# Optimization experiments

Measured on AMD Instinct MI355X. Metric: run time of the kernel, lower is better.

The kernel has to match this reference:

```python
import jax, jax.numpy as jnp
import numpy as np

B, H, W, C = 2, 64, 64, 96
DIN, NST, RNK, K = 192, 16, 6, 4
L = H * W


def _make_ids():
    idx = np.arange(L).reshape(H, W)
    p0 = idx.reshape(-1)
    p1 = idx.T.reshape(-1)
    p2 = p0[::-1].copy()
    p3 = p1[::-1].copy()
    scan = np.stack([p0, p1, p2, p3]).astype(np.int32)
    inv = np.stack([np.argsort(p) for p in scan]).astype(np.int32)
    return jnp.asarray(scan), jnp.asarray(inv)


def setup_inputs() -> dict:
    key = jax.random.key(0)
    ks = jax.random.split(key, 10)
    scan_ids, inv_ids = _make_ids()
    std = RNK ** -0.5
    # dt bias init: inverse-softplus of dt ~ LogUniform(1e-3, 1e-1), as in VMM.dt_init
    u = jax.random.uniform(ks[5], (K, DIN))
    dt = jnp.exp(u * (np.log(0.1) - np.log(0.001)) + np.log(0.001))
    dt_b = dt + jnp.log(-jnp.expm1(-dt))
    return {
        "x": jax.random.normal(ks[0], (B, H, W, C), jnp.float32),
        "W_in": jax.random.normal(ks[1], (2 * DIN, C), jnp.float32) * 0.02,
        "conv_w": jax.random.normal(ks[2], (DIN, 1, 3, 3), jnp.float32) * 0.1,
        "conv_b": jnp.zeros((DIN,), jnp.float32),
        "x_proj_w": jax.random.normal(ks[3], (K, RNK + 2 * NST, DIN), jnp.float32) * 0.02,
        "dt_w": jax.random.uniform(ks[4], (K, DIN, RNK), jnp.float32, -std, std),
        "dt_b": dt_b.astype(jnp.float32),
        "A_logs": jnp.log(jnp.tile(jnp.arange(1, NST + 1, dtype=jnp.float32)[None], (K * DIN, 1))),
        "Ds": jnp.ones((K * DIN,), jnp.float32),
        "gate_w": jax.random.normal(ks[6], (4 * DIN, 4), jnp.float32) * 0.1,  # grouped 1x1 conv, groups=DIN
        "gate_b": jnp.zeros((4 * DIN,), jnp.float32),
        "ln_g": jnp.ones((DIN,), jnp.float32),
        "ln_b": jnp.zeros((DIN,), jnp.float32),
        "W_out": jax.random.normal(ks[7], (C, DIN), jnp.float32) * 0.02,
        "scan_ids": scan_ids,
        "inv_ids": inv_ids,
    }


def _forward(x, W_in, conv_w, conv_b, x_proj_w, dt_w, dt_b, A_logs, Ds, gate_w, gate_b, ln_g, ln_b, W_out, scan_ids, inv_ids):
    b, h, w, c = x.shape
    l = h * w
    din = conv_w.shape[0]
    k = x_proj_w.shape[0]
    nst = A_logs.shape[1]
    rnk = dt_w.shape[2]
    # in_proj + split into x / gate z
    xz = x @ W_in.T
    xc, z = jnp.split(xz, 2, axis=-1)
    xc = jnp.transpose(xc, (0, 3, 1, 2))  # (b, din, h, w)
    # depthwise 3x3 conv + SiLU
    xc = jax.lax.conv_general_dilated(
        xc, conv_w, (1, 1), "SAME", feature_group_count=din,
        dimension_numbers=("NCHW", "OIHW", "NCHW")) + conv_b[None, :, None, None]
    xc = jax.nn.silu(xc)
    # multi-directional gather (mair_ids_scan)
    xf = xc.reshape(b, din, l)
    xs = jnp.moveaxis(xf[:, :, scan_ids], 2, 1)  # (b, k, din, l)
    # x_proj (grouped 1x1 conv) -> dt, B, C
    x_dbl = jnp.einsum("bkdl,krd->bkrl", xs, x_proj_w)
    dts, Bs, Cs = jnp.split(x_dbl, [rnk, rnk + nst], axis=2)  # (b,k,rnk,l),(b,k,n,l),(b,k,n,l)
    delta = jax.nn.softplus(jnp.einsum("bkrl,kdr->bkdl", dts, dt_w) + dt_b[None, :, :, None])
    A = -jnp.exp(A_logs).reshape(k, din, nst)
    dA = jnp.exp(delta[..., None] * A[None, :, :, None, :])              # (b,k,d,l,n)
    dBu = (delta * xs)[..., None] * jnp.moveaxis(Bs, 2, 3)[:, :, None]   # (b,k,d,l,n)

    def step(hst, inp):
        da, dbu = inp
        hst = da * hst + dbu
        return hst, hst

    h0 = jnp.zeros((b, k, din, nst), jnp.float32)
    _, hs = jax.lax.scan(step, h0, (jnp.moveaxis(dA, 3, 0), jnp.moveaxis(dBu, 3, 0)))  # (l,b,k,d,n)
    ys = jnp.einsum("lbkdn,bknl->bkdl", hs, Cs) + xs * Ds.reshape(k, din)[None, :, :, None]
    # inverse scatter (mair_ids_inverse) + concat along channels
    y = jax.vmap(lambda yk, ik: yk[..., ik], in_axes=(1, 0), out_axes=1)(ys, inv_ids)
    y = y.reshape(b, k * din, h, w)
    # ShuffleAttn gating: group = din, group_channels = k
    shuf = y.reshape(b, k, din, h, w).transpose(0, 2, 1, 3, 4).reshape(b, k * din, h, w)
    pooled = shuf.mean(axis=(2, 3)).reshape(b, din, k)
    gate = jax.nn.sigmoid(jnp.einsum("bgi,goi->bgo", pooled, gate_w.reshape(din, k, k)) + gate_b.reshape(din, k))
    gate = gate.transpose(0, 2, 1).reshape(b, k * din)  # channel_rearrange
    y = y * gate[:, :, None, None]
    # sum the 4 direction branches
    y = y.reshape(b, k, din, h, w).sum(axis=1)
    y = jnp.transpose(y, (0, 2, 3, 1))  # (b,h,w,din)
    # LayerNorm(d_inner)
    mu = y.mean(-1, keepdims=True)
    var = ((y - mu) ** 2).mean(-1, keepdims=True)
    y = (y - mu) / jnp.sqrt(var + 1e-5) * ln_g + ln_b
    y = y * jax.nn.silu(z)
    return y @ W_out.T


def reference(x, W_in, conv_w, conv_b, x_proj_w, dt_w, dt_b, A_logs, Ds, gate_w, gate_b, ln_g, ln_b, W_out, scan_ids, inv_ids):
    return _forward(x, W_in, conv_w, conv_b, x_proj_w, dt_w, dt_b, A_logs, Ds, gate_w, gate_b, ln_g, ln_b, W_out, scan_ids, inv_ids)
```

## Files before the change

### kernel.cpp

```cpp
#include <hip/hip_runtime.h>
#include <math.h>

#define BB 2
#define CC 96
#define DIN 192
#define NST 16
#define RNK 6
#define KK 4
#define LL 4096
#define RTOT (RNK + 2*NST)


__global__ __launch_bounds__(256) void k_inproj(const float* __restrict__ x,
        const float* __restrict__ W_in, float* __restrict__ xc_pre,
        float* __restrict__ z_silu) {
    __shared__ float lx[96*65];
    __shared__ float wt[48*196];
    int b = blockIdx.y, z = blockIdx.z;
    int l0 = blockIdx.x * 64;
    int t = threadIdx.x;
    for (int i = 0; i < 24; ++i) {
        int e = t + 256*i;
        int l = e / 96, c = e % 96;
        lx[c*65 + l] = x[((size_t)(b*LL + l0 + l))*96 + c];
    }
    int lg = t & 15;
    int og = t >> 4;
    float acc[4][12];
    #pragma unroll
    for (int j = 0; j < 4; ++j)
        #pragma unroll
        for (int q = 0; q < 12; ++q) acc[j][q] = 0.f;
    for (int p = 0; p < 2; ++p) {
        __syncthreads();
        for (int i = 0; i < 36; ++i) {
            int e = t + 256*i;
            int cc = e % 48, oc = e / 48;
            wt[cc*196 + oc] = W_in[((size_t)(z*192 + oc))*96 + p*48 + cc];
        }
        __syncthreads();
        #pragma unroll 2
        for (int cc = 0; cc < 48; ++cc) {
            int c = p*48 + cc;
            float x0 = lx[c*65 + 4*lg + 0];
            float x1 = lx[c*65 + 4*lg + 1];
            float x2 = lx[c*65 + 4*lg + 2];
            float x3 = lx[c*65 + 4*lg + 3];
            const float* wr = &wt[cc*196 + 12*og];
            float4 w0 = *(const float4*)(wr);
            float4 w1 = *(const float4*)(wr + 4);
            float4 w2 = *(const float4*)(wr + 8);
            float wv[12] = {w0.x,w0.y,w0.z,w0.w, w1.x,w1.y,w1.z,w1.w,
                            w2.x,w2.y,w2.z,w2.w};
            #pragma unroll
            for (int q = 0; q < 12; ++q) {
                acc[0][q] += x0*wv[q];
                acc[1][q] += x1*wv[q];
                acc[2][q] += x2*wv[q];
                acc[3][q] += x3*wv[q];
            }
        }
    }
    float* dst = (z == 0) ? xc_pre : z_silu;
    #pragma unroll
    for (int j = 0; j < 4; ++j) {
        int l = l0 + 4*lg + j;
        size_t base = (size_t)(b*LL + l)*DIN + 12*og;
        #pragma unroll
        for (int q = 0; q < 12; ++q) {
            float v = acc[j][q];
            if (z) v = v / (1.f + __expf(-v));
            dst[base + q] = v;
        }
    }
}

__global__ __launch_bounds__(256) void k_conv(const float* __restrict__ xc,
        const float* __restrict__ cw, const float* __restrict__ cb,
        float* __restrict__ out) {
    int gid = blockIdx.x*256 + threadIdx.x;
    int d = gid % DIN;
    int r = gid / DIN;
    int l = r & 4095, b = r >> 12;
    int w = l & 63, h = l >> 6;
    float acc = cb[d];
    #pragma unroll
    for (int dh = -1; dh <= 1; ++dh) {
        int h2 = h + dh;
        bool okh = (h2 >= 0) && (h2 < 64);
        #pragma unroll
        for (int dw = -1; dw <= 1; ++dw) {
            int w2 = w + dw;
            if (okh && w2 >= 0 && w2 < 64)
                acc += xc[((size_t)(b*LL + h2*64 + w2))*DIN + d] * cw[d*9 + (dh+1)*3 + (dw+1)];
        }
    }
    out[((size_t)(b*LL + l))*DIN + d] = acc / (1.f + __expf(-acc));
}

__global__ __launch_bounds__(512) void k_proj(const float* __restrict__ xconv,
        const int* __restrict__ scan_ids, const float* __restrict__ xpw,
        float* __restrict__ dts, float* __restrict__ Bs, float* __restrict__ Cs) {
    __shared__ float lxs[96*65];
    __shared__ float lw[RTOT*96];
    __shared__ float lbc[64*33];
    __shared__ int lsid[64];
    int k = blockIdx.y, b = blockIdx.z;
    int l0 = blockIdx.x * 64;
    int t = threadIdx.x;
    if (t < 64) lsid[t] = scan_ids[k*LL + l0 + t];
    int l = t & 63;
    int rg = __builtin_amdgcn_readfirstlane(t >> 6);
    float acc[5];
    #pragma unroll
    for (int j = 0; j < 5; ++j) acc[j] = 0.f;
    for (int p = 0; p < 2; ++p) {
        __syncthreads();
        for (int i = 0; i < 12; ++i) {
            int e = t + 512*i;
            int dd = e % 96, ll = e / 96;
            lxs[dd*65 + ll] = xconv[((size_t)(b*LL + lsid[ll]))*DIN + p*96 + dd];
        }
        for (int i = 0; i < 8; ++i) {
            int e = t + 512*i;
            if (e < RTOT*96) {
                int r = e / 96, dd = e % 96;
                lw[r*96 + dd] = xpw[(size_t)k*RTOT*DIN + r*DIN + p*96 + dd];
            }
        }
        __syncthreads();
        for (int dd = 0; dd < 96; dd += 4) {
            float x0 = lxs[(dd+0)*65 + l];
            float x1 = lxs[(dd+1)*65 + l];
            float x2 = lxs[(dd+2)*65 + l];
            float x3 = lxs[(dd+3)*65 + l];
            #pragma unroll
            for (int j = 0; j < 5; ++j) {
                int r = rg + 8*j;
                if (r < RTOT) {
                    float4 w = *(const float4*)&lw[r*96 + dd];
                    acc[j] += x0*w.x + x1*w.y + x2*w.z + x3*w.w;
                }
            }
        }
    }
    int bk = b*KK + k;
    #pragma unroll
    for (int j = 0; j < 5; ++j) {
        int r = rg + 8*j;
        if (r < RNK)       dts[((size_t)bk*LL + l0 + l)*8 + r] = acc[j];
        else if (r < RTOT) lbc[l*33 + (r - RNK)] = acc[j];
    }
    __syncthreads();
    size_t rowb = ((size_t)bk*LL + l0)*NST;
    for (int i = 0; i < 2; ++i) {
        int e = t + 512*i;
        int n = e & 15, ll = e >> 4;
        Bs[rowb + ll*NST + n] = lbc[ll*33 + n];
        Cs[rowb + ll*NST + n] = lbc[ll*33 + 16 + n];
    }
}

__global__ __launch_bounds__(384) void k_scan1(const float* __restrict__ xconv,
        const float* __restrict__ Bs, const float* __restrict__ dts,
        const float* __restrict__ dtw, const float* __restrict__ dtb,
        const int* __restrict__ scan_ids, const float* __restrict__ A_logs,
        float* __restrict__ segA, float* __restrict__ segB, int SL) {
    __shared__ float ldel[32*DIN];
    __shared__ float lB[32*NST];
    __shared__ int lsid[256];
    int seg = blockIdx.x, bk = blockIdx.y;
    int b = bk >> 2, k = bk & 3;
    int t = threadIdx.x;
    int half = t & 1, d = t >> 1;
    int l0 = seg * SL;
    for (int i = t; i < SL; i += 384) lsid[i] = scan_ids[k*LL + l0 + i];
    float Av[8];
    {
        const float4* ap = (const float4*)(A_logs + ((k*DIN + d)*NST + half*8));
        float4 a0 = ap[0], a1 = ap[1];
        Av[0]=-__expf(a0.x); Av[1]=-__expf(a0.y); Av[2]=-__expf(a0.z); Av[3]=-__expf(a0.w);
        Av[4]=-__expf(a1.x); Av[5]=-__expf(a1.y); Av[6]=-__expf(a1.z); Av[7]=-__expf(a1.w);
    }
    float Av0 = -__expf(A_logs[(k*DIN + d)*NST]);
    bool okl = true;
    #pragma unroll
    for (int q = 0; q < 8; ++q) {
        float m = (float)(half*8 + q + 1);
        okl = okl && (fabsf(Av[q] - m*Av0) <= 1e-4f*m);
    }
    int fast = __all(okl);
    int dd = t % DIN, li0 = t / DIN;
    float wdt[RNK];
    float bdt = dtb[k*DIN + dd];
    #pragma unroll
    for (int r = 0; r < RNK; ++r) wdt[r] = dtw[(k*DIN + dd)*RNK + r];
    float h[8];
    #pragma unroll
    for (int n = 0; n < 8; ++n) h[n] = 0.f;
    float sumdv = 0.f;
    __syncthreads();
    float xn = xconv[((size_t)(b*LL + lsid[0]))*DIN + d];
    for (int c0 = 0; c0 < SL; c0 += 32) {
        for (int li = li0; li < 32; li += 2) {
            const float* dr = dts + ((size_t)bk*LL + l0 + c0 + li)*8;
            float aa = bdt;
            #pragma unroll
            for (int r = 0; r < RNK; ++r) aa += dr[r]*wdt[r];
            ldel[li*DIN + dd] = fmaxf(aa, 0.f) + __logf(1.f + __expf(-fabsf(aa)));
        }
        for (int e = t; e < 32*NST; e += 384)
            lB[e] = Bs[((size_t)bk*LL + l0 + c0)*NST + e];
        __syncthreads();
        if (fast) {
            for (int li2 = 0; li2 < 32; ++li2) {
                int li = c0 + li2;
                float xv = xn;
                if (li + 1 < SL) xn = xconv[((size_t)(b*LL + lsid[li+1]))*DIN + d];
                float dv = ldel[li2*DIN + d];
                sumdv += dv;
                float dxv = dv * xv;
                float4 b0 = *(const float4*)&lB[li2*NST + half*8];
                float4 b1 = *(const float4*)&lB[li2*NST + half*8 + 4];
                float bb[8] = {b0.x,b0.y,b0.z,b0.w, b1.x,b1.y,b1.z,b1.w};
                float P[8];
                float E1 = __expf(dv * Av0);
                P[0] = E1;       P[1] = E1*E1;   P[2] = P[1]*E1; P[3] = P[1]*P[1];
                P[4] = P[3]*E1;  P[5] = P[2]*P[2]; P[6] = P[5]*E1; P[7] = P[3]*P[3];
                float s = half ? P[7] : 1.0f;
                #pragma unroll
                for (int n = 0; n < 8; ++n)
                    h[n] = (s*P[n])*h[n] + dxv*bb[n];
            }
        } else {
            for (int li2 = 0; li2 < 32; ++li2) {
                int li = c0 + li2;
                float xv = xn;
                if (li + 1 < SL) xn = xconv[((size_t)(b*LL + lsid[li+1]))*DIN + d];
                float dv = ldel[li2*DIN + d];
                sumdv += dv;
                float dxv = dv * xv;
                float4 b0 = *(const float4*)&lB[li2*NST + half*8];
                float4 b1 = *(const float4*)&lB[li2*NST + half*8 + 4];
                float bb[8] = {b0.x,b0.y,b0.z,b0.w, b1.x,b1.y,b1.z,b1.w};
                #pragma unroll
                for (int n = 0; n < 8; ++n) {
                    float e2 = __expf(dv * Av[n]);
                    h[n] = e2*h[n] + dxv*bb[n];
                }
            }
        }
        __syncthreads();
    }
    float a[8];
    #pragma unroll
    for (int n = 0; n < 8; ++n) a[n] = __expf(Av[n]*sumdv);
    size_t base = (((size_t)bk*gridDim.x + seg)*DIN + d)*NST + half*8;
    *(float4*)&segA[base]     = make_float4(a[0],a[1],a[2],a[3]);
    *(float4*)&segA[base + 4] = make_float4(a[4],a[5],a[6],a[7]);
    *(float4*)&segB[base]     = make_float4(h[0],h[1],h[2],h[3]);
    *(float4*)&segB[base + 4] = make_float4(h[4],h[5],h[6],h[7]);
}

__global__ __launch_bounds__(256) void k_scan2(const float* __restrict__ segA,
        const float* __restrict__ segB, float* __restrict__ hinit, int SEGC) {
    int idx = blockIdx.x*256 + threadIdx.x;
    if (idx >= BB*KK*DIN*NST) return;
    int bk = idx / (DIN*NST);
    int dn = idx % (DIN*NST);
    const size_t stride = DIN*NST;
    size_t o = (size_t)bk*SEGC*stride + dn;
    float h = 0.f;
    for (int s = 0; s < SEGC; s += 8) {
        float av[8], bv[8];
        #pragma unroll
        for (int j = 0; j < 8; ++j) {
            av[j] = segA[o + j*stride];
            bv[j] = segB[o + j*stride];
        }
        #pragma unroll
        for (int j = 0; j < 8; ++j) {
            hinit[o + j*stride] = h;
            h = av[j]*h + bv[j];
        }
        o += 8*stride;
    }
}

__global__ __launch_bounds__(384) void k_scan3(const float* __restrict__ xconv,
        const float* __restrict__ Bs, const float* __restrict__ Cs,
        const float* __restrict__ dts, const float* __restrict__ dtw,
        const float* __restrict__ dtb,
        const int* __restrict__ scan_ids, const float* __restrict__ A_logs,
        const float* __restrict__ Ds, const float* __restrict__ hinit,
        float* __restrict__ y_dirs, float* __restrict__ poolsum, int SL) {
    __shared__ float ldel[32*DIN];
    __shared__ float lB[32*NST];
    __shared__ float lC[32*NST];
    __shared__ int lsid[256];
    int seg = blockIdx.x, bk = blockIdx.y;
    int b = bk >> 2, k = bk & 3;
    int t = threadIdx.x;
    int half = t & 1, d = t >> 1;
    int l0 = seg * SL;
    for (int i = t; i < SL; i += 384) lsid[i] = scan_ids[k*LL + l0 + i];
    float Av[8];
    {
        const float4* ap = (const float4*)(A_logs + ((k*DIN + d)*NST + half*8));
        float4 a0 = ap[0], a1 = ap[1];
        Av[0]=-__expf(a0.x); Av[1]=-__expf(a0.y); Av[2]=-__expf(a0.z); Av[3]=-__expf(a0.w);
        Av[4]=-__expf(a1.x); Av[5]=-__expf(a1.y); Av[6]=-__expf(a1.z); Av[7]=-__expf(a1.w);
    }
    float Av0 = -__expf(A_logs[(k*DIN + d)*NST]);
    bool okl = true;
    #pragma unroll
    for (int q = 0; q < 8; ++q) {
        float m = (float)(half*8 + q + 1);
        okl = okl && (fabsf(Av[q] - m*Av0) <= 1e-4f*m);
    }
    int fast = __all(okl);
    float Dv = Ds[k*DIN + d];
    int dd = t % DIN, li0 = t / DIN;
    float wdt[RNK];
    float bdt = dtb[k*DIN + dd];
    #pragma unroll
    for (int r = 0; r < RNK; ++r) wdt[r] = dtw[(k*DIN + dd)*RNK + r];
    float h[8];
    {
        size_t base = (((size_t)bk*gridDim.x + seg)*DIN + d)*NST + half*8;
        float4 h0 = *(const float4*)&hinit[base];
        float4 h1 = *(const float4*)&hinit[base + 4];
        h[0]=h0.x; h[1]=h0.y; h[2]=h0.z; h[3]=h0.w;
        h[4]=h1.x; h[5]=h1.y; h[6]=h1.z; h[7]=h1.w;
    }
    __syncthreads();
    float xn = xconv[((size_t)(b*LL + lsid[0]))*DIN + d];
    float pool = 0.f;
    for (int c0 = 0; c0 < SL; c0 += 32) {
        for (int li = li0; li < 32; li += 2) {
            const float* dr = dts + ((size_t)bk*LL + l0 + c0 + li)*8;
            float aa = bdt;
            #pragma unroll
            for (int r = 0; r < RNK; ++r) aa += dr[r]*wdt[r];
            ldel[li*DIN + dd] = fmaxf(aa, 0.f) + __logf(1.f + __expf(-fabsf(aa)));
        }
        for (int e = t; e < 32*NST; e += 384) {
            lB[e] = Bs[((size_t)bk*LL + l0 + c0)*NST + e];
            lC[e] = Cs[((size_t)bk*LL + l0 + c0)*NST + e];
        }
        __syncthreads();
        for (int li2 = 0; li2 < 32; ++li2) {
            int li = c0 + li2;
            int l = lsid[li];
            float xv = xn;
            if (li + 1 < SL) xn = xconv[((size_t)(b*LL + lsid[li+1]))*DIN + d];
            float dv = ldel[li2*DIN + d];
            float dxv = dv * xv;
            float4 b0 = *(const float4*)&lB[li2*NST + half*8];
            float4 b1 = *(const float4*)&lB[li2*NST + half*8 + 4];
            float4 c0v = *(const float4*)&lC[li2*NST + half*8];
            float4 c1v = *(const float4*)&lC[li2*NST + half*8 + 4];
            float bb[8] = {b0.x,b0.y,b0.z,b0.w, b1.x,b1.y,b1.z,b1.w};
            float cc[8] = {c0v.x,c0v.y,c0v.z,c0v.w, c1v.x,c1v.y,c1v.z,c1v.w};
            float y = 0.f;
            if (fast) {
                float P[8];
                float E1 = __expf(dv * Av0);
                P[0] = E1;       P[1] = E1*E1;     P[2] = P[1]*E1; P[3] = P[1]*P[1];
                P[4] = P[3]*E1;  P[5] = P[2]*P[2]; P[6] = P[5]*E1; P[7] = P[3]*P[3];
                float s = half ? P[7] : 1.0f;
                #pragma unroll
                for (int n = 0; n < 8; ++n) {
                    h[n] = (s*P[n])*h[n] + dxv*bb[n];
                    y += h[n]*cc[n];
                }
            } else {
                #pragma unroll
                for (int n = 0; n < 8; ++n) {
                    float e2 = __expf(dv * Av[n]);
                    h[n] = e2*h[n] + dxv*bb[n];
                    y += h[n]*cc[n];
                }
            }
            y += __shfl_xor(y, 1);
            if (half == 0) {
                y += xv * Dv;
                y_dirs[((size_t)(bk*LL + l))*DIN + d] = y;
                pool += y;
            }
        }
        __syncthreads();
    }
    if (half == 0) atomicAdd(&poolsum[(b*DIN + d)*KK + k], pool);
}

__global__ __launch_bounds__(256) void k_final(const float* __restrict__ y_dirs,
        const float* __restrict__ poolsum, const float* __restrict__ gw,
        const float* __restrict__ gb, const float* __restrict__ z_silu,
        const float* __restrict__ lng, const float* __restrict__ lnb,
        const float* __restrict__ Wout, float* __restrict__ out) {
    __shared__ float buf[16*193];
    __shared__ float lgate[DIN*KK];
    __shared__ float lmu[16], lrs[16];
    int b = blockIdx.y;
    int l0 = blockIdx.x * 16;
    int t = threadIdx.x;
    for (int e = t; e < DIN*KK; e += 256) {
        int d = e >> 2, o = e & 3;
        float acc = gb[d*KK + o];
        #pragma unroll
        for (int i = 0; i < KK; ++i)
            acc += (poolsum[(b*DIN + d)*KK + i] * (1.f/LL)) * gw[(d*KK + o)*KK + i];
        lgate[d*KK + o] = 1.f/(1.f + __expf(-acc));
    }
    __syncthreads();
    for (int i = 0; i < 12; ++i) {
        int e = t + 256*i;
        int d = e % DIN, l = e / DIN;
        float acc = 0.f;
        #pragma unroll
        for (int k = 0; k < KK; ++k)
            acc += y_dirs[((size_t)((b*KK + k)*LL + l0 + l))*DIN + d] * lgate[d*KK + k];
        buf[l*193 + d] = acc;
    }
    __syncthreads();
    int l2 = t >> 4, q = t & 15;
    float s = 0.f, s2 = 0.f;
    for (int i = 0; i < 12; ++i) {
        float v = buf[l2*193 + q + 16*i];
        s += v; s2 += v*v;
    }
    s += __shfl_xor(s, 1);  s2 += __shfl_xor(s2, 1);
    s += __shfl_xor(s, 2);  s2 += __shfl_xor(s2, 2);
    s += __shfl_xor(s, 4);  s2 += __shfl_xor(s2, 4);
    s += __shfl_xor(s, 8);  s2 += __shfl_xor(s2, 8);
    if (q == 0) {
        float mu = s * (1.f/DIN);
        float var = s2 * (1.f/DIN) - mu*mu;
        lmu[l2] = mu;
        lrs[l2] = rsqrtf(var + 1e-5f);
    }
    __syncthreads();
    for (int i = 0; i < 12; ++i) {
        int e = t + 256*i;
        int d = e % DIN, l = e / DIN;
        float v = buf[l*193 + d];
        float tv = (v - lmu[l]) * lrs[l] * lng[d] + lnb[d];
        tv *= z_silu[((size_t)(b*LL + l0 + l))*DIN + d];
        buf[l*193 + d] = tv;
    }
    __syncthreads();
    int l = t & 15;
    int c0 = (t >> 4) * 6;
    float acc[6];
    #pragma unroll
    for (int cc = 0; cc < 6; ++cc) acc[cc] = 0.f;
    for (int d = 0; d < DIN; ++d) {
        float v = buf[l*193 + d];
        #pragma unroll
        for (int cc = 0; cc < 6; ++cc)
            acc[cc] += v * Wout[(c0 + cc)*DIN + d];
    }
    #pragma unroll
    for (int cc = 0; cc < 6; ++cc)
        out[((size_t)(b*LL + l0 + l))*CC + c0 + cc] = acc[cc];
}

extern "C" void kernel_launch(void* const* d_in, const int* in_sizes, int n_in,
                              void* d_out, int out_size, void* d_ws, size_t ws_size,
                              hipStream_t stream) {
    const float* x      = (const float*)d_in[0];
    const float* W_in   = (const float*)d_in[1];
    const float* conv_w = (const float*)d_in[2];
    const float* conv_b = (const float*)d_in[3];
    const float* xpw    = (const float*)d_in[4];
    const float* dt_w   = (const float*)d_in[5];
    const float* dt_b   = (const float*)d_in[6];
    const float* A_logs = (const float*)d_in[7];
    const float* Ds     = (const float*)d_in[8];
    const float* gate_w = (const float*)d_in[9];
    const float* gate_b = (const float*)d_in[10];
    const float* ln_g   = (const float*)d_in[11];
    const float* ln_b   = (const float*)d_in[12];
    const float* W_out  = (const float*)d_in[13];
    const int* scan_ids = (const int*)d_in[14];
    float* out = (float*)d_out;

    const size_t baseF = 6291456ull + 2ull*1572864 + 262144ull + 2ull*524288 + 3072;
    int SEGC = 16;
    if ((baseF + 3ull*128*24576)*4 <= ws_size) SEGC = 128;
    else if ((baseF + 3ull*64*24576)*4 <= ws_size) SEGC = 64;
    else if ((baseF + 3ull*32*24576)*4 <= ws_size) SEGC = 32;
    int SL = LL / SEGC;
    size_t segF = (size_t)SEGC * 24576;

    float* ws      = (float*)d_ws;
    float* y_dirs  = ws;
    float* xc_pre  = ws;
    float* z_silu  = y_dirs  + 6291456;
    float* xconv   = z_silu  + 1572864;
    float* dts     = xconv   + 1572864;
    float* Bs      = dts     + 262144;
    float* Cs      = Bs      + 524288;
    float* poolsum = Cs      + 524288;
    float* segA    = poolsum + 3072;
    float* segB    = segA    + segF;
    float* hinit   = segB    + segF;

    hipMemsetAsync(poolsum, 0, 1536*sizeof(float), stream);

    k_inproj<<<dim3(LL/64, BB, 2), 256, 0, stream>>>(x, W_in, xc_pre, z_silu);
    k_conv<<<(BB*DIN*LL)/256, 256, 0, stream>>>(xc_pre, conv_w, conv_b, xconv);
    k_proj<<<dim3(LL/64, KK, BB), 512, 0, stream>>>(xconv, scan_ids, xpw,
                                                    dts, Bs, Cs);
    k_scan1<<<dim3(SEGC, BB*KK), 384, 0, stream>>>(xconv, Bs, dts, dt_w, dt_b,
                                                   scan_ids, A_logs, segA, segB, SL);
    k_scan2<<<(BB*KK*DIN*NST + 255)/256, 256, 0, stream>>>(segA, segB, hinit, SEGC);
    k_scan3<<<dim3(SEGC, BB*KK), 384, 0, stream>>>(xconv, Bs, Cs, dts, dt_w, dt_b,
                                                   scan_ids, A_logs, Ds, hinit,
                                                   y_dirs, poolsum, SL);
    k_final<<<dim3(LL/16, BB), 256, 0, stream>>>(y_dirs, poolsum, gate_w, gate_b,
                                                 z_silu, ln_g, ln_b, W_out, out);
}
```

Measured before the change: 283.0 us.

## Compute local-scan outputs in first pass and add carry-in correction in apply kernel

The chunked selective scan is restructured. The first pass now runs the full local scan from a zero state and writes partial outputs y plus the segment summaries. A new lightweight apply kernel then adds the carry-in contribution C·exp(A·cumΔ)·h_init, using a Horner-style polynomial when A is an integer multiple of A0. This removes the second full recurrence pass over B and x, at the cost of an extra read-modify-write of y_dirs. hinit aliases segA in place, which shrinks workspace needs. The first pass loses the fast power-chain path and always calls exp per state, and the apply correction may be less accurate for long segments.

Measured after the change: 277.9 us. Within noise of the previous version (-1.8%).

```diff
diff --git a/kernel.cpp b/kernel.cpp
--- a/kernel.cpp
+++ b/kernel.cpp
@@ -162,138 +162,13 @@
 }
 
 __global__ __launch_bounds__(384) void k_scan1(const float* __restrict__ xconv,
-        const float* __restrict__ Bs, const float* __restrict__ dts,
-        const float* __restrict__ dtw, const float* __restrict__ dtb,
-        const int* __restrict__ scan_ids, const float* __restrict__ A_logs,
-        float* __restrict__ segA, float* __restrict__ segB, int SL) {
-    __shared__ float ldel[32*DIN];
-    __shared__ float lB[32*NST];
-    __shared__ int lsid[256];
-    int seg = blockIdx.x, bk = blockIdx.y;
-    int b = bk >> 2, k = bk & 3;
-    int t = threadIdx.x;
-    int half = t & 1, d = t >> 1;
-    int l0 = seg * SL;
-    for (int i = t; i < SL; i += 384) lsid[i] = scan_ids[k*LL + l0 + i];
-    float Av[8];
-    {
-        const float4* ap = (const float4*)(A_logs + ((k*DIN + d)*NST + half*8));
-        float4 a0 = ap[0], a1 = ap[1];
-        Av[0]=-__expf(a0.x); Av[1]=-__expf(a0.y); Av[2]=-__expf(a0.z); Av[3]=-__expf(a0.w);
-        Av[4]=-__expf(a1.x); Av[5]=-__expf(a1.y); Av[6]=-__expf(a1.z); Av[7]=-__expf(a1.w);
-    }
-    float Av0 = -__expf(A_logs[(k*DIN + d)*NST]);
-    bool okl = true;
-    #pragma unroll
-    for (int q = 0; q < 8; ++q) {
-        float m = (float)(half*8 + q + 1);
-        okl = okl && (fabsf(Av[q] - m*Av0) <= 1e-4f*m);
-    }
-    int fast = __all(okl);
-    int dd = t % DIN, li0 = t / DIN;
-    float wdt[RNK];
-    float bdt = dtb[k*DIN + dd];
-    #pragma unroll
-    for (int r = 0; r < RNK; ++r) wdt[r] = dtw[(k*DIN + dd)*RNK + r];
-    float h[8];
-    #pragma unroll
-    for (int n = 0; n < 8; ++n) h[n] = 0.f;
-    float sumdv = 0.f;
-    __syncthreads();
-    float xn = xconv[((size_t)(b*LL + lsid[0]))*DIN + d];
-    for (int c0 = 0; c0 < SL; c0 += 32) {
-        for (int li = li0; li < 32; li += 2) {
-            const float* dr = dts + ((size_t)bk*LL + l0 + c0 + li)*8;
-            float aa = bdt;
-            #pragma unroll
-            for (int r = 0; r < RNK; ++r) aa += dr[r]*wdt[r];
-            ldel[li*DIN + dd] = fmaxf(aa, 0.f) + __logf(1.f + __expf(-fabsf(aa)));
-        }
-        for (int e = t; e < 32*NST; e += 384)
-            lB[e] = Bs[((size_t)bk*LL + l0 + c0)*NST + e];
-        __syncthreads();
-        if (fast) {
-            for (int li2 = 0; li2 < 32; ++li2) {
-                int li = c0 + li2;
-                float xv = xn;
-                if (li + 1 < SL) xn = xconv[((size_t)(b*LL + lsid[li+1]))*DIN + d];
-                float dv = ldel[li2*DIN + d];
-                sumdv += dv;
-                float dxv = dv * xv;
-                float4 b0 = *(const float4*)&lB[li2*NST + half*8];
-                float4 b1 = *(const float4*)&lB[li2*NST + half*8 + 4];
-                float bb[8] = {b0.x,b0.y,b0.z,b0.w, b1.x,b1.y,b1.z,b1.w};
-                float P[8];
-                float E1 = __expf(dv * Av0);
-                P[0] = E1;       P[1] = E1*E1;   P[2] = P[1]*E1; P[3] = P[1]*P[1];
-                P[4] = P[3]*E1;  P[5] = P[2]*P[2]; P[6] = P[5]*E1; P[7] = P[3]*P[3];
-                float s = half ? P[7] : 1.0f;
-                #pragma unroll
-                for (int n = 0; n < 8; ++n)
-                    h[n] = (s*P[n])*h[n] + dxv*bb[n];
-            }
-        } else {
-            for (int li2 = 0; li2 < 32; ++li2) {
-                int li = c0 + li2;
-                float xv = xn;
-                if (li + 1 < SL) xn = xconv[((size_t)(b*LL + lsid[li+1]))*DIN + d];
-                float dv = ldel[li2*DIN + d];
-                sumdv += dv;
-                float dxv = dv * xv;
-                float4 b0 = *(const float4*)&lB[li2*NST + half*8];
-                float4 b1 = *(const float4*)&lB[li2*NST + half*8 + 4];
-                float bb[8] = {b0.x,b0.y,b0.z,b0.w, b1.x,b1.y,b1.z,b1.w};
-                #pragma unroll
-                for (int n = 0; n < 8; ++n) {
-                    float e2 = __expf(dv * Av[n]);
-                    h[n] = e2*h[n] + dxv*bb[n];
-                }
-            }
-        }
-        __syncthreads();
-    }
-    float a[8];
-    #pragma unroll
-    for (int n = 0; n < 8; ++n) a[n] = __expf(Av[n]*sumdv);
-    size_t base = (((size_t)bk*gridDim.x + seg)*DIN + d)*NST + half*8;
-    *(float4*)&segA[base]     = make_float4(a[0],a[1],a[2],a[3]);
-    *(float4*)&segA[base + 4] = make_float4(a[4],a[5],a[6],a[7]);
-    *(float4*)&segB[base]     = make_float4(h[0],h[1],h[2],h[3]);
-    *(float4*)&segB[base + 4] = make_float4(h[4],h[5],h[6],h[7]);
-}
-
-__global__ __launch_bounds__(256) void k_scan2(const float* __restrict__ segA,
-        const float* __restrict__ segB, float* __restrict__ hinit, int SEGC) {
-    int idx = blockIdx.x*256 + threadIdx.x;
-    if (idx >= BB*KK*DIN*NST) return;
-    int bk = idx / (DIN*NST);
-    int dn = idx % (DIN*NST);
-    const size_t stride = DIN*NST;
-    size_t o = (size_t)bk*SEGC*stride + dn;
-    float h = 0.f;
-    for (int s = 0; s < SEGC; s += 8) {
-        float av[8], bv[8];
-        #pragma unroll
-        for (int j = 0; j < 8; ++j) {
-            av[j] = segA[o + j*stride];
-            bv[j] = segB[o + j*stride];
-        }
-        #pragma unroll
-        for (int j = 0; j < 8; ++j) {
-            hinit[o + j*stride] = h;
-            h = av[j]*h + bv[j];
-        }
-        o += 8*stride;
-    }
-}
-
-__global__ __launch_bounds__(384) void k_scan3(const float* __restrict__ xconv,
         const float* __restrict__ Bs, const float* __restrict__ Cs,
         const float* __restrict__ dts, const float* __restrict__ dtw,
         const float* __restrict__ dtb,
         const int* __restrict__ scan_ids, const float* __restrict__ A_logs,
-        const float* __restrict__ Ds, const float* __restrict__ hinit,
-        float* __restrict__ y_dirs, float* __restrict__ poolsum, int SL) {
+        const float* __restrict__ Ds,
+        float* __restrict__ y_dirs, float* __restrict__ segA,
+        float* __restrict__ segB, int SL) {
     __shared__ float ldel[32*DIN];
     __shared__ float lB[32*NST];
     __shared__ float lC[32*NST];
@@ -311,14 +186,6 @@
         Av[0]=-__expf(a0.x); Av[1]=-__expf(a0.y); Av[2]=-__expf(a0.z); Av[3]=-__expf(a0.w);
         Av[4]=-__expf(a1.x); Av[5]=-__expf(a1.y); Av[6]=-__expf(a1.z); Av[7]=-__expf(a1.w);
     }
-    float Av0 = -__expf(A_logs[(k*DIN + d)*NST]);
-    bool okl = true;
-    #pragma unroll
-    for (int q = 0; q < 8; ++q) {
-        float m = (float)(half*8 + q + 1);
-        okl = okl && (fabsf(Av[q] - m*Av0) <= 1e-4f*m);
-    }
-    int fast = __all(okl);
     float Dv = Ds[k*DIN + d];
     int dd = t % DIN, li0 = t / DIN;
     float wdt[RNK];
@@ -326,16 +193,11 @@
     #pragma unroll
     for (int r = 0; r < RNK; ++r) wdt[r] = dtw[(k*DIN + dd)*RNK + r];
     float h[8];
-    {
-        size_t base = (((size_t)bk*gridDim.x + seg)*DIN + d)*NST + half*8;
-        float4 h0 = *(const float4*)&hinit[base];
-        float4 h1 = *(const float4*)&hinit[base + 4];
-        h[0]=h0.x; h[1]=h0.y; h[2]=h0.z; h[3]=h0.w;
-        h[4]=h1.x; h[5]=h1.y; h[6]=h1.z; h[7]=h1.w;
-    }
+    #pragma unroll
+    for (int n = 0; n < 8; ++n) h[n] = 0.f;
+    float sumdv = 0.f;
     __syncthreads();
     float xn = xconv[((size_t)(b*LL + lsid[0]))*DIN + d];
-    float pool = 0.f;
     for (int c0 = 0; c0 < SL; c0 += 32) {
         for (int li = li0; li < 32; li += 2) {
             const float* dr = dts + ((size_t)bk*LL + l0 + c0 + li)*8;
@@ -355,6 +217,7 @@
             float xv = xn;
             if (li + 1 < SL) xn = xconv[((size_t)(b*LL + lsid[li+1]))*DIN + d];
             float dv = ldel[li2*DIN + d];
+            sumdv += dv;
             float dxv = dv * xv;
             float4 b0 = *(const float4*)&lB[li2*NST + half*8];
             float4 b1 = *(const float4*)&lB[li2*NST + half*8 + 4];
@@ -363,29 +226,141 @@
             float bb[8] = {b0.x,b0.y,b0.z,b0.w, b1.x,b1.y,b1.z,b1.w};
             float cc[8] = {c0v.x,c0v.y,c0v.z,c0v.w, c1v.x,c1v.y,c1v.z,c1v.w};
             float y = 0.f;
-            if (fast) {
-                float P[8];
-                float E1 = __expf(dv * Av0);
-                P[0] = E1;       P[1] = E1*E1;     P[2] = P[1]*E1; P[3] = P[1]*P[1];
-                P[4] = P[3]*E1;  P[5] = P[2]*P[2]; P[6] = P[5]*E1; P[7] = P[3]*P[3];
-                float s = half ? P[7] : 1.0f;
-                #pragma unroll
-                for (int n = 0; n < 8; ++n) {
-                    h[n] = (s*P[n])*h[n] + dxv*bb[n];
-                    y += h[n]*cc[n];
-                }
-            } else {
-                #pragma unroll
-                for (int n = 0; n < 8; ++n) {
-                    float e2 = __expf(dv * Av[n]);
-                    h[n] = e2*h[n] + dxv*bb[n];
-                    y += h[n]*cc[n];
-                }
+            #pragma unroll
+            for (int n = 0; n < 8; ++n) {
+                float e2 = __expf(dv * Av[n]);
+                h[n] = e2*h[n] + dxv*bb[n];
+                y += h[n]*cc[n];
             }
             y += __shfl_xor(y, 1);
             if (half == 0) {
                 y += xv * Dv;
                 y_dirs[((size_t)(bk*LL + l))*DIN + d] = y;
+            }
+        }
+        __syncthreads();
+    }
+    float a[8];
+    #pragma unroll
+    for (int n = 0; n < 8; ++n) a[n] = __expf(Av[n]*sumdv);
+    size_t base = (((size_t)bk*gridDim.x + seg)*DIN + d)*NST + half*8;
+    *(float4*)&segA[base]     = make_float4(a[0],a[1],a[2],a[3]);
+    *(float4*)&segA[base + 4] = make_float4(a[4],a[5],a[6],a[7]);
+    *(float4*)&segB[base]     = make_float4(h[0],h[1],h[2],h[3]);
+    *(float4*)&segB[base + 4] = make_float4(h[4],h[5],h[6],h[7]);
+}
+
+__global__ __launch_bounds__(256) void k_scan2(const float* segA,
+        const float* segB, float* hinit, int SEGC) {
+    int idx = blockIdx.x*256 + threadIdx.x;
+    if (idx >= BB*KK*DIN*NST) return;
+    int bk = idx / (DIN*NST);
+    int dn = idx % (DIN*NST);
+    const size_t stride = DIN*NST;
+    size_t o = (size_t)bk*SEGC*stride + dn;
+    float h = 0.f;
+    for (int s = 0; s < SEGC; s += 8) {
+        float av[8], bv[8];
+        #pragma unroll
+        for (int j = 0; j < 8; ++j) {
+            av[j] = segA[o + j*stride];
+            bv[j] = segB[o + j*stride];
+        }
+        #pragma unroll
+        for (int j = 0; j < 8; ++j) {
+            hinit[o + j*stride] = h;
+            h = av[j]*h + bv[j];
+        }
+        o += 8*stride;
+    }
+}
+
+__global__ __launch_bounds__(384) void k_apply(const float* __restrict__ Cs,
+        const float* __restrict__ dts, const float* __restrict__ dtw,
+        const float* __restrict__ dtb,
+        const int* __restrict__ scan_ids, const float* __restrict__ A_logs,
+        const float* __restrict__ hinit,
+        float* __restrict__ y_dirs, float* __restrict__ poolsum, int SL) {
+    __shared__ float ldel[32*DIN];
+    __shared__ float lC[32*NST];
+    __shared__ int lsid[256];
+    int seg = blockIdx.x, bk = blockIdx.y;
+    int b = bk >> 2, k = bk & 3;
+    int t = threadIdx.x;
+    int half = t & 1, d = t >> 1;
+    int l0 = seg * SL;
+    for (int i = t; i < SL; i += 384) lsid[i] = scan_ids[k*LL + l0 + i];
+    float Av[8];
+    {
+        const float4* ap = (const float4*)(A_logs + ((k*DIN + d)*NST + half*8));
+        float4 a0 = ap[0], a1 = ap[1];
+        Av[0]=-__expf(a0.x); Av[1]=-__expf(a0.y); Av[2]=-__expf(a0.z); Av[3]=-__expf(a0.w);
+        Av[4]=-__expf(a1.x); Av[5]=-__expf(a1.y); Av[6]=-__expf(a1.z); Av[7]=-__expf(a1.w);
+    }
+    float Av0 = -__expf(A_logs[(k*DIN + d)*NST]);
+    bool okl = true;
+    #pragma unroll
+    for (int q = 0; q < 8; ++q) {
+        float m = (float)(half*8 + q + 1);
+        okl = okl && (fabsf(Av[q] - m*Av0) <= 1e-4f*m);
+    }
+    int fast = __all(okl);
+    float h0[8];
+    {
+        size_t base = (((size_t)bk*gridDim.x + seg)*DIN + d)*NST + half*8;
+        float4 v0 = *(const float4*)&hinit[base];
+        float4 v1 = *(const float4*)&hinit[base + 4];
+        h0[0]=v0.x; h0[1]=v0.y; h0[2]=v0.z; h0[3]=v0.w;
+        h0[4]=v1.x; h0[5]=v1.y; h0[6]=v1.z; h0[7]=v1.w;
+    }
+    int dd = t % DIN, li0 = t / DIN;
+    float wdt[RNK];
+    float bdt = dtb[k*DIN + dd];
+    #pragma unroll
+    for (int r = 0; r < RNK; ++r) wdt[r] = dtw[(k*DIN + dd)*RNK + r];
+    float cum = 0.f;
+    float pool = 0.f;
+    __syncthreads();
+    for (int c0 = 0; c0 < SL; c0 += 32) {
+        for (int li = li0; li < 32; li += 2) {
+            const float* dr = dts + ((size_t)bk*LL + l0 + c0 + li)*8;
+            float aa = bdt;
+            #pragma unroll
+            for (int r = 0; r < RNK; ++r) aa += dr[r]*wdt[r];
+            ldel[li*DIN + dd] = fmaxf(aa, 0.f) + __logf(1.f + __expf(-fabsf(aa)));
+        }
+        for (int e = t; e < 32*NST; e += 384)
+            lC[e] = Cs[((size_t)bk*LL + l0 + c0)*NST + e];
+        __syncthreads();
+        for (int li2 = 0; li2 < 32; ++li2) {
+            int li = c0 + li2;
+            int l = lsid[li];
+            cum += ldel[li2*DIN + d];
+            float4 c0v = *(const float4*)&lC[li2*NST + half*8];
+            float4 c1v = *(const float4*)&lC[li2*NST + half*8 + 4];
+            float cc[8] = {c0v.x,c0v.y,c0v.z,c0v.w, c1v.x,c1v.y,c1v.z,c1v.w};
+            float g;
+            if (fast) {
+                float E = __expf(Av0 * cum);
+                g = 0.f;
+                #pragma unroll
+                for (int q = 7; q >= 0; --q) g = g*E + cc[q]*h0[q];
+                g *= E;
+                if (half) {
+                    float E2 = E*E, E4 = E2*E2;
+                    g *= E4*E4;
+                }
+            } else {
+                g = 0.f;
+                #pragma unroll
+                for (int q = 0; q < 8; ++q)
+                    g += cc[q]*h0[q]*__expf(Av[q]*cum);
+            }
+            g += __shfl_xor(g, 1);
+            if (half == 0) {
+                size_t yo = ((size_t)(bk*LL + l))*DIN + d;
+                float y = y_dirs[yo] + g;
+                y_dirs[yo] = y;
                 pool += y;
             }
         }
@@ -488,9 +463,9 @@
 
     const size_t baseF = 6291456ull + 2ull*1572864 + 262144ull + 2ull*524288 + 3072;
     int SEGC = 16;
-    if ((baseF + 3ull*128*24576)*4 <= ws_size) SEGC = 128;
-    else if ((baseF + 3ull*64*24576)*4 <= ws_size) SEGC = 64;
-    else if ((baseF + 3ull*32*24576)*4 <= ws_size) SEGC = 32;
+    if ((baseF + 2ull*128*24576)*4 <= ws_size) SEGC = 128;
+    else if ((baseF + 2ull*64*24576)*4 <= ws_size) SEGC = 64;
+    else if ((baseF + 2ull*32*24576)*4 <= ws_size) SEGC = 32;
     int SL = LL / SEGC;
     size_t segF = (size_t)SEGC * 24576;
 
@@ -505,7 +480,7 @@
     float* poolsum = Cs      + 524288;
     float* segA    = poolsum + 3072;
     float* segB    = segA    + segF;
-    float* hinit   = segB    + segF;
+    float* hinit   = segA;
 
     hipMemsetAsync(poolsum, 0, 1536*sizeof(float), stream);
 
@@ -513,11 +488,12 @@
     k_conv<<<(BB*DIN*LL)/256, 256, 0, stream>>>(xc_pre, conv_w, conv_b, xconv);
     k_proj<<<dim3(LL/64, KK, BB), 512, 0, stream>>>(xconv, scan_ids, xpw,
                                                     dts, Bs, Cs);
-    k_scan1<<<dim3(SEGC, BB*KK), 384, 0, stream>>>(xconv, Bs, dts, dt_w, dt_b,
-                                                   scan_ids, A_logs, segA, segB, SL);
+    k_scan1<<<dim3(SEGC, BB*KK), 384, 0, stream>>>(xconv, Bs, Cs, dts, dt_w, dt_b,
+                                                   scan_ids, A_logs, Ds,
+                                                   y_dirs, segA, segB, SL);
     k_scan2<<<(BB*KK*DIN*NST + 255)/256, 256, 0, stream>>>(segA, segB, hinit, SEGC);
-    k_scan3<<<dim3(SEGC, BB*KK), 384, 0, stream>>>(xconv, Bs, Cs, dts, dt_w, dt_b,
-                                                   scan_ids, A_logs, Ds, hinit,
+    k_apply<<<dim3(SEGC, BB*KK), 384, 0, stream>>>(Cs, dts, dt_w, dt_b,
+                                                   scan_ids, A_logs, hinit,
                                                    y_dirs, poolsum, SL);
     k_final<<<dim3(LL/16, BB), 256, 0, stream>>>(y_dirs, poolsum, gate_w, gate_b,
                                                  z_silu, ln_g, ln_b, W_out, out);
```
